# Performance work log

Measured on AMD Instinct MI355X. Metric: run time of the kernel, lower is better.

The kernel has to match this reference:

```python
import jax, jax.numpy as jnp
import numpy as np
import math

B, S, H = 2, 2048, 1024
NH, HD = 16, 64
MAX_SCALE = 4


def setup_inputs() -> dict:
    key = jax.random.key(0)
    ks = jax.random.split(key, 8)
    s = 0.02
    return {
        "x": jax.random.normal(ks[0], (B, S, H), dtype=jnp.float32),
        "Wqkv": jax.random.normal(ks[1], (H, 3 * H), dtype=jnp.float32) * s,
        "bqkv": jnp.zeros((3 * H,), dtype=jnp.float32),
        "Wout": jax.random.normal(ks[2], (H, H), dtype=jnp.float32) * s,
        "bout": jnp.zeros((H,), dtype=jnp.float32),
        "Wscale": jax.random.normal(ks[3], (H, MAX_SCALE), dtype=jnp.float32) * s,
        "bscale": jnp.zeros((MAX_SCALE,), dtype=jnp.float32),
    }


def reference(x, Wqkv, bqkv, Wout, bout, Wscale, bscale):
    b, s, h = x.shape
    inv_sqrt_hd = 1.0 / math.sqrt(HD)
    # qkv projection -> [3, b, nh, s, hd]
    qkv = (x @ Wqkv + bqkv).reshape(b, s, 3, NH, HD).transpose(2, 0, 3, 1, 4)
    q, k, v = qkv[0], qkv[1], qkv[2]
    # per-token soft weights over scales [b, s, max_scale]
    scale_weights = jax.nn.softmax(x @ Wscale + bscale, axis=-1)
    out = jnp.zeros((b, NH, s, HD), dtype=x.dtype)
    for scale_idx in range(MAX_SCALE):
        dilation = 2 ** scale_idx
        kd = k[:, :, ::dilation]  # strided (dilated) gather of keys
        vd = v[:, :, ::dilation]
        scores = jnp.einsum("bhqd,bhkd->bhqk", q, kd) * inv_sqrt_hd
        attn = jax.nn.softmax(scores, axis=-1)
        o = jnp.einsum("bhqk,bhkd->bhqd", attn, vd)
        w = scale_weights[:, :, scale_idx][:, None, :, None]  # [b,1,s,1]
        out = out + o * w
    out = out.transpose(0, 2, 1, 3).reshape(b, s, h)
    return out @ Wout + bout
```

## Files before the change

kernel.cpp:

```cpp
#include <hip/hip_runtime.h>
#include <stdint.h>

typedef unsigned short u16;
typedef __attribute__((ext_vector_type(8))) __bf16 bf8v;
typedef __attribute__((ext_vector_type(4))) float f4v;
typedef __attribute__((ext_vector_type(16))) float f16v;
typedef __attribute__((ext_vector_type(4))) uint32_t u32x4;

#define BB 2
#define SS 2048
#define HH 1024

#define OFF_Q   0u
#define OFF_K0  8388608u
#define OFF_V0  24117248u
#define OFF_V1  32505856u
#define OFF_V2  36700160u
#define OFF_V3  38797312u
#define OFF_WQT 39845888u
#define OFF_WOT 46137344u
#define OFF_XB  48234496u
#define OFF_SCW 56623104u

__device__ __forceinline__ u16 f2bf(float f) {
    union { float f; uint32_t u; } v; v.f = f;
    uint32_t r = v.u + 0x7fffu + ((v.u >> 16) & 1u);
    return (u16)(r >> 16);
}
__device__ __forceinline__ uint32_t pk2(float a, float b) {
    return (uint32_t)f2bf(a) | ((uint32_t)f2bf(b) << 16);
}
__device__ __forceinline__ uint32_t pkt2(float a, float b) {
    union { float f; uint32_t u; } x, y; x.f = a; y.f = b;
    return (x.u >> 16) | (y.u & 0xffff0000u);
}

__global__ __launch_bounds__(256) void xconv_kernel(const float* __restrict__ x,
                                                    u16* __restrict__ xb) {
    size_t t = (size_t)blockIdx.x * 256 + threadIdx.x;
    float4 v = *(const float4*)&x[t * 4];
    uint2 pk; pk.x = pk2(v.x, v.y); pk.y = pk2(v.z, v.w);
    *(uint2*)&xb[t * 4] = pk;
}

__global__ __launch_bounds__(256) void wconv_kernel(const float* __restrict__ W,
                                                    u16* __restrict__ Wt,
                                                    int N, int K) {
    __shared__ float tile[64][69];
    const int tid = threadIdx.x;
    const int n0 = blockIdx.x * 64, k0 = blockIdx.y * 64;
    const int r = tid >> 4, c4 = (tid & 15) * 4;
#pragma unroll
    for (int it = 0; it < 4; it++) {
        float4 v = *(const float4*)&W[(size_t)(k0 + it * 16 + r) * N + n0 + c4];
        tile[it * 16 + r][c4 + 0] = v.x; tile[it * 16 + r][c4 + 1] = v.y;
        tile[it * 16 + r][c4 + 2] = v.z; tile[it * 16 + r][c4 + 3] = v.w;
    }
    __syncthreads();
#pragma unroll
    for (int it = 0; it < 4; it++) {
        int n = it * 16 + r;
        uint2 pk;
        pk.x = pk2(tile[c4 + 0][n], tile[c4 + 1][n]);
        pk.y = pk2(tile[c4 + 2][n], tile[c4 + 3][n]);
        *(uint2*)&Wt[(size_t)(n0 + n) * K + k0 + c4] = pk;
    }
}

__global__ __launch_bounds__(256) void scale_kernel(const float* __restrict__ x,
                                                    const float* __restrict__ Wscale,
                                                    const float* __restrict__ bscale,
                                                    float* __restrict__ scw) {
    const int lane = threadIdx.x & 63;
    const int wid  = threadIdx.x >> 6;
    const int row  = blockIdx.x * 4 + wid;
    float a0 = 0.f, a1 = 0.f, a2 = 0.f, a3 = 0.f;
    for (int i = 0; i < 16; i++) {
        int hh = lane + i * 64;
        float xs = x[(size_t)row * HH + hh];
        float4 wv = *(const float4*)&Wscale[hh * 4];
        a0 += xs * wv.x; a1 += xs * wv.y; a2 += xs * wv.z; a3 += xs * wv.w;
    }
    for (int off = 1; off < 64; off <<= 1) {
        a0 += __shfl_xor(a0, off); a1 += __shfl_xor(a1, off);
        a2 += __shfl_xor(a2, off); a3 += __shfl_xor(a3, off);
    }
    if (lane == 0) {
        a0 += bscale[0]; a1 += bscale[1]; a2 += bscale[2]; a3 += bscale[3];
        float mx = fmaxf(fmaxf(a0, a1), fmaxf(a2, a3));
        float e0 = __expf(a0 - mx), e1 = __expf(a1 - mx);
        float e2 = __expf(a2 - mx), e3 = __expf(a3 - mx);
        float inv = 1.f / (e0 + e1 + e2 + e3);
        float4 o = {e0 * inv, e1 * inv, e2 * inv, e3 * inv};
        *(float4*)&scw[(size_t)row * 4] = o;
    }
}

template<int MODE>
__global__ __launch_bounds__(256) void gemm_bt(const u16* __restrict__ A,
                                               const u16* __restrict__ Bt,
                                               const float* __restrict__ bias,
                                               void* __restrict__ Cp,
                                               int N, int K) {
    __shared__ __align__(16) u16 At[128 * 40];
    __shared__ __align__(16) u16 Btl[128 * 40];
    const int tid  = threadIdx.x;
    const int lane = tid & 63;
    const int wid  = tid >> 6;
    const int l15  = lane & 15;
    const int quad = lane >> 4;
    const int wm = wid & 1, wn = wid >> 1;
    const int m0 = blockIdx.y * 128;
    const int n0 = blockIdx.x * 128;
    const int srow = tid >> 2;
    const int sc8  = (tid & 3) * 8;

    f4v acc[4][4];
#pragma unroll
    for (int i = 0; i < 4; i++)
#pragma unroll
        for (int j = 0; j < 4; j++) acc[i][j] = (f4v){0.f, 0.f, 0.f, 0.f};

    uint4 pa0 = *(const uint4*)(A  + (size_t)(m0 + srow) * K + sc8);
    uint4 pa1 = *(const uint4*)(A  + (size_t)(m0 + srow + 64) * K + sc8);
    uint4 pb0 = *(const uint4*)(Bt + (size_t)(n0 + srow) * K + sc8);
    uint4 pb1 = *(const uint4*)(Bt + (size_t)(n0 + srow + 64) * K + sc8);

    for (int kc = 0; kc < K; kc += 32) {
        __syncthreads();
        *(uint4*)&At[srow * 40 + sc8]         = pa0;
        *(uint4*)&At[(srow + 64) * 40 + sc8]  = pa1;
        *(uint4*)&Btl[srow * 40 + sc8]        = pb0;
        *(uint4*)&Btl[(srow + 64) * 40 + sc8] = pb1;
        __syncthreads();
        if (kc + 32 < K) {
            pa0 = *(const uint4*)(A  + (size_t)(m0 + srow) * K + kc + 32 + sc8);
            pa1 = *(const uint4*)(A  + (size_t)(m0 + srow + 64) * K + kc + 32 + sc8);
            pb0 = *(const uint4*)(Bt + (size_t)(n0 + srow) * K + kc + 32 + sc8);
            pb1 = *(const uint4*)(Bt + (size_t)(n0 + srow + 64) * K + kc + 32 + sc8);
        }
        bf8v af[4], bf[4];
#pragma unroll
        for (int t = 0; t < 4; t++) {
            af[t] = *(const bf8v*)&At[(wm * 64 + t * 16 + l15) * 40 + quad * 8];
            bf[t] = *(const bf8v*)&Btl[(wn * 64 + t * 16 + l15) * 40 + quad * 8];
        }
#pragma unroll
        for (int ti = 0; ti < 4; ti++)
#pragma unroll
            for (int tj = 0; tj < 4; tj++)
                acc[ti][tj] = __builtin_amdgcn_mfma_f32_16x16x32_bf16(af[ti], bf[tj], acc[ti][tj], 0, 0, 0);
    }

    if (MODE == 0) {
#pragma unroll
        for (int ti = 0; ti < 4; ti++)
#pragma unroll
            for (int tj = 0; tj < 4; tj++)
#pragma unroll
                for (int r = 0; r < 4; r++) {
                    int m = m0 + wm * 64 + ti * 16 + quad * 4 + r;
                    int n = n0 + wn * 64 + tj * 16 + l15;
                    ((float*)Cp)[(size_t)m * N + n] = acc[ti][tj][r] + bias[n];
                }
    } else {
        char* ws = (char*)Cp;
        u16* Qd = (u16*)ws;
        u16* K0 = (u16*)(ws + OFF_K0);
        u16* V0 = (u16*)(ws + OFF_V0); u16* V1 = (u16*)(ws + OFF_V1);
        u16* V2 = (u16*)(ws + OFF_V2); u16* V3 = (u16*)(ws + OFF_V3);
        const int region = n0 >> 10;
        if (region == 0) {
#pragma unroll
            for (int ti = 0; ti < 4; ti++)
#pragma unroll
                for (int tj = 0; tj < 4; tj++)
#pragma unroll
                    for (int r = 0; r < 4; r++) {
                        int m = m0 + wm * 64 + ti * 16 + quad * 4 + r;
                        int n = n0 + wn * 64 + tj * 16 + l15;
                        Qd[(size_t)m * 1024 + n] = f2bf(acc[ti][tj][r] + bias[n]);
                    }
        } else if (region == 1) {
#pragma unroll
            for (int ti = 0; ti < 4; ti++)
#pragma unroll
                for (int tj = 0; tj < 4; tj++) {
                    int n  = n0 + wn * 64 + tj * 16 + l15;
                    int nk = n - 1024;
                    int h = nk >> 6, hd = nk & 63;
#pragma unroll
                    for (int r = 0; r < 4; r++) {
                        int m = m0 + wm * 64 + ti * 16 + quad * 4 + r;
                        int bb = m >> 11, tok = m & 2047;
                        int bh = bb * 16 + h;
                        u16 bv = f2bf((acc[ti][tj][r] + bias[n]) * 0.18033688f);
                        K0[((size_t)bh * 2048 + tok) * 64 + hd] = bv;
                    }
                }
        } else {
#pragma unroll
            for (int ti = 0; ti < 4; ti++)
#pragma unroll
                for (int tj = 0; tj < 4; tj++) {
                    int n  = n0 + wn * 64 + tj * 16 + l15;
                    int nv = n - 2048;
                    int h = nv >> 6, hd = nv & 63;
                    int tokb = m0 + wm * 64 + ti * 16 + quad * 4;
                    int bb = tokb >> 11, tok = tokb & 2047;
                    int bh = bb * 16 + h;
                    float v0 = acc[ti][tj][0] + bias[n];
                    float v1 = acc[ti][tj][1] + bias[n];
                    float v2 = acc[ti][tj][2] + bias[n];
                    float v3 = acc[ti][tj][3] + bias[n];
                    u16 c0 = f2bf(v0), c1 = f2bf(v1), c2 = f2bf(v2), c3 = f2bf(v3);
                    uint2 pk;
                    pk.x = (uint32_t)c0 | ((uint32_t)c1 << 16);
                    pk.y = (uint32_t)c2 | ((uint32_t)c3 << 16);
                    int tokp = (tok & ~15) | ((tok & 4) << 1) | ((tok & 8) >> 1);
                    *(uint2*)&V0[((size_t)bh * 64 + hd) * 2048 + tokp] = pk;
                    int kk = tok >> 1;
                    int v1p = (kk & ~15) | ((kk & 2) << 2) | ((kk & 12) >> 1);
                    *(uint32_t*)&V1[((size_t)bh * 64 + hd) * 1024 + v1p] =
                        (uint32_t)c0 | ((uint32_t)c2 << 16);
                    int t2 = tok >> 2;
                    int v2i = (t2 & ~15) | ((t2 & 1) << 3) | ((t2 & 15) >> 1);
                    V2[((size_t)bh * 64 + hd) * 512 + v2i] = c0;
                    if (!(quad & 1)) V3[((size_t)bh * 64 + hd) * 256 + (tok >> 3)] = c0;
                }
        }
    }
}

__global__ __launch_bounds__(256, 2) void attn_kernel(const char* __restrict__ ws) {
    __shared__ __align__(16) u16 smem[15872];
    u16* Kt0  = smem;
    u16* Kt1  = smem + 2304;
    u16* Vt0  = smem + 4608;
    u16* Vt1  = smem + 7168;
    u16* V1t0 = smem + 9728;
    u16* V1t1 = smem + 11264;
    u16* V2t  = smem + 12800;
    u16* V3t  = smem + 14336;

    const u16* Qd    = (const u16*)(ws + OFF_Q);
    const float* scw = (const float*)(ws + OFF_SCW);
    u16* attnb       = (u16*)(ws + OFF_Q);

    const int tid  = threadIdx.x;
    const int lane = tid & 63;
    const int wid  = tid >> 6;
    const int l31  = lane & 31;
    const int half = lane >> 5;
    const int b = blockIdx.z, h = blockIdx.y;
    const int q  = blockIdx.x * 128 + wid * 32 + l31;
    const int bh = b * 16 + h;

    const int skey = tid >> 3;
    const int shd8 = (tid & 7) * 8;
    const int svhd = tid >> 2;
    const int svk8 = (tid & 3) * 8;
    const int vi4  = (tid & 3) * 4;

    bf8v qf[4];
#pragma unroll
    for (int ks = 0; ks < 4; ks++)
        qf[ks] = *(const bf8v*)(Qd + (size_t)(b * SS + q) * 1024 + h * 64 + ks * 16 + half * 8);

    const u16* Kb  = (const u16*)(ws + OFF_K0) + (size_t)bh * (2048 * 64);
    const u16* Vb0 = (const u16*)(ws + OFF_V0) + (size_t)bh * (64 * 2048);
    const u16* Vb1 = (const u16*)(ws + OFF_V1) + (size_t)bh * (64 * 1024);
    const u16* Vb2 = (const u16*)(ws + OFF_V2) + (size_t)bh * (64 * 512);
    const u16* Vb3 = (const u16*)(ws + OFF_V3) + (size_t)bh * (64 * 256);

    f16v oacc0[2], oacc1[2], oacc2[2], oacc3[2];
#pragma unroll
    for (int ht = 0; ht < 2; ht++)
#pragma unroll
        for (int r = 0; r < 16; r++) {
            oacc0[ht][r] = 0.f; oacc1[ht][r] = 0.f;
            oacc2[ht][r] = 0.f; oacc3[ht][r] = 0.f;
        }
    float ls0 = 0.f, ls1 = 0.f, ls2 = 0.f, ls3 = 0.f;

    uint4 kr  = *(const uint4*)(Kb + (size_t)skey * 64 + shd8);
    uint4 vr  = *(const uint4*)(Vb0 + (size_t)svhd * 2048 + svk8);
    uint2 v1r = *(const uint2*)(Vb1 + (size_t)svhd * 1024 + vi4);
    uint2 v2r = *(const uint2*)(Vb2 + (size_t)svhd * 512 + vi4);
    uint2 v3r = *(const uint2*)(Vb3 + (size_t)svhd * 256 + vi4);
    *(uint4*)&Kt0[skey * 72 + shd8] = kr;
    *(uint4*)&Vt0[svhd * 40 + svk8] = vr;
    *(uint2*)&V1t0[svhd * 24 + vi4] = v1r;
    kr  = *(const uint4*)(Kb + (size_t)(32 + skey) * 64 + shd8);
    vr  = *(const uint4*)(Vb0 + (size_t)svhd * 2048 + 32 + svk8);
    v1r = *(const uint2*)(Vb1 + (size_t)svhd * 1024 + 16 + vi4);
    __syncthreads();

    uint32_t Pa[4], Pb[4];
    union uu { u32x4 u; bf8v b; };

    for (int cc = 0; cc < 64; cc += 4) {
#pragma unroll
        for (int ph = 0; ph < 4; ph++) {
            const int c = cc + ph;
            u16* Ktc  = (ph & 1) ? Kt1 : Kt0;
            u16* Vtc  = (ph & 1) ? Vt1 : Vt0;
            u16* V1tc = (ph & 1) ? V1t1 : V1t0;
            u16* Ktn  = (ph & 1) ? Kt0 : Kt1;
            u16* Vtn  = (ph & 1) ? Vt0 : Vt1;
            u16* V1tn = (ph & 1) ? V1t0 : V1t1;

            f16v sa;
#pragma unroll
            for (int r = 0; r < 16; r++) sa[r] = 0.f;
#pragma unroll
            for (int ks = 0; ks < 4; ks++) {
                bf8v ka = *(const bf8v*)&Ktc[l31 * 72 + ks * 16 + half * 8];
                sa = __builtin_amdgcn_mfma_f32_32x32x16_bf16(ka, qf[ks], sa, 0, 0, 0);
            }
            float e[16];
#pragma unroll
            for (int g = 0; g < 4; g++) {
                float e0 = exp2f(sa[g * 4 + 0]);
                float e1 = exp2f(sa[g * 4 + 1]);
                float e2 = exp2f(sa[g * 4 + 2]);
                float e3 = exp2f(sa[g * 4 + 3]);
                e[g * 4 + 0] = e0; e[g * 4 + 1] = e1;
                e[g * 4 + 2] = e2; e[g * 4 + 3] = e3;
                ls0 += (e0 + e1) + (e2 + e3);
                ls1 += e0 + e2;
                ls2 += e0;
                if (!half) ls3 += e0;
            }
            uint32_t F00 = pkt2(e[0],  e[1]),  F01 = pkt2(e[2],  e[3]);
            uint32_t F02 = pkt2(e[4],  e[5]),  F03 = pkt2(e[6],  e[7]);
            uint32_t F10 = pkt2(e[8],  e[9]),  F11 = pkt2(e[10], e[11]);
            uint32_t F12 = pkt2(e[12], e[13]), F13 = pkt2(e[14], e[15]);
            uint32_t G0 = pkt2(e[0],  e[2]),   G1 = pkt2(e[4],  e[6]);
            uint32_t G2 = pkt2(e[8],  e[10]),  G3 = pkt2(e[12], e[14]);
            Pa[ph] = pkt2(e[0], e[4]);
            Pb[ph] = pkt2(e[8], e[12]);

            if (c + 1 < 64) {
                *(uint4*)&Ktn[skey * 72 + shd8] = kr;
                *(uint4*)&Vtn[svhd * 40 + svk8] = vr;
                *(uint2*)&V1tn[svhd * 24 + vi4] = v1r;
            }
            if (!(ph & 1)) {
                *(uint2*)&V2t[svhd * 24 + vi4] = v2r;
                if (ph == 0)
                    *(uint2*)&V3t[svhd * 24 + vi4] = v3r;
            }
            if (c + 2 < 64) {
                kr  = *(const uint4*)(Kb + (size_t)((c + 2) * 32 + skey) * 64 + shd8);
                vr  = *(const uint4*)(Vb0 + (size_t)svhd * 2048 + (c + 2) * 32 + svk8);
                v1r = *(const uint2*)(Vb1 + (size_t)svhd * 1024 + (c + 2) * 16 + vi4);
                if (!((c + 2) & 1))
                    v2r = *(const uint2*)(Vb2 + (size_t)svhd * 512 + (c + 2) * 8 + vi4);
                if (!((c + 2) & 3))
                    v3r = *(const uint2*)(Vb3 + (size_t)svhd * 256 + (c + 2) * 4 + vi4);
            }
            {
                uu p0; p0.u = (u32x4){F00, F01, F02, F03};
#pragma unroll
                for (int ht = 0; ht < 2; ht++) {
                    bf8v va = *(const bf8v*)&Vtc[(ht * 32 + l31) * 40 + half * 8];
                    oacc0[ht] = __builtin_amdgcn_mfma_f32_32x32x16_bf16(va, p0.b, oacc0[ht], 0, 0, 0);
                }
                uu p1; p1.u = (u32x4){F10, F11, F12, F13};
#pragma unroll
                for (int ht = 0; ht < 2; ht++) {
                    bf8v va = *(const bf8v*)&Vtc[(ht * 32 + l31) * 40 + 16 + half * 8];
                    oacc0[ht] = __builtin_amdgcn_mfma_f32_32x32x16_bf16(va, p1.b, oacc0[ht], 0, 0, 0);
                }
            }
            {
                uu ps; ps.u = (u32x4){G0, G1, G2, G3};
#pragma unroll
                for (int ht = 0; ht < 2; ht++) {
                    bf8v va1 = *(const bf8v*)&V1tc[(ht * 32 + l31) * 24 + half * 8];
                    oacc1[ht] = __builtin_amdgcn_mfma_f32_32x32x16_bf16(va1, ps.b, oacc1[ht], 0, 0, 0);
                }
            }
            if (ph == 1 || ph == 3) {
                uu p2; p2.u = (u32x4){Pa[ph - 1], Pb[ph - 1], Pa[ph], Pb[ph]};
#pragma unroll
                for (int ht = 0; ht < 2; ht++) {
                    bf8v va2 = *(const bf8v*)&V2t[(ht * 32 + l31) * 24 + half * 8];
                    oacc2[ht] = __builtin_amdgcn_mfma_f32_32x32x16_bf16(va2, p2.b, oacc2[ht], 0, 0, 0);
                }
            }
            if (ph == 3) {
                uint32_t t0 = __shfl_xor(Pa[2], 32);
                uint32_t t1 = __shfl_xor(Pb[2], 32);
                uint32_t t2 = __shfl_xor(Pa[3], 32);
                uint32_t t3 = __shfl_xor(Pb[3], 32);
                uint32_t w0 = half ? t0 : Pa[0];
                uint32_t w1 = half ? t1 : Pb[0];
                uint32_t w2 = half ? t2 : Pa[1];
                uint32_t w3 = half ? t3 : Pb[1];
                uu p3; p3.u = (u32x4){w0, w1, w2, w3};
#pragma unroll
                for (int ht = 0; ht < 2; ht++) {
                    bf8v va3 = *(const bf8v*)&V3t[(ht * 32 + l31) * 24 + half * 8];
                    oacc3[ht] = __builtin_amdgcn_mfma_f32_32x32x16_bf16(va3, p3.b, oacc3[ht], 0, 0, 0);
                }
            }
            __syncthreads();
        }
    }
    ls0 += __shfl_xor(ls0, 32);
    ls1 += __shfl_xor(ls1, 32);
    ls2 += __shfl_xor(ls2, 32);
    ls3 += __shfl_xor(ls3, 32);
    float4 sw = *(const float4*)&scw[(size_t)(b * SS + q) * 4];
    float w0 = sw.x / ls0, w1 = sw.y / ls1, w2 = sw.z / ls2, w3 = sw.w / ls3;

    const size_t base = (size_t)(b * SS + q) * 1024 + h * 64;
#pragma unroll
    for (int ht = 0; ht < 2; ht++)
#pragma unroll
        for (int g = 0; g < 4; g++) {
            float f0 = w0 * oacc0[ht][g * 4 + 0] + w1 * oacc1[ht][g * 4 + 0]
                     + w2 * oacc2[ht][g * 4 + 0] + w3 * oacc3[ht][g * 4 + 0];
            float f1 = w0 * oacc0[ht][g * 4 + 1] + w1 * oacc1[ht][g * 4 + 1]
                     + w2 * oacc2[ht][g * 4 + 1] + w3 * oacc3[ht][g * 4 + 1];
            float f2 = w0 * oacc0[ht][g * 4 + 2] + w1 * oacc1[ht][g * 4 + 2]
                     + w2 * oacc2[ht][g * 4 + 2] + w3 * oacc3[ht][g * 4 + 2];
            float f3 = w0 * oacc0[ht][g * 4 + 3] + w1 * oacc1[ht][g * 4 + 3]
                     + w2 * oacc2[ht][g * 4 + 3] + w3 * oacc3[ht][g * 4 + 3];
            uint2 pk;
            pk.x = pk2(f0, f1);
            pk.y = pk2(f2, f3);
            *(uint2*)&attnb[base + ht * 32 + g * 8 + half * 4] = pk;
        }
}

extern "C" void kernel_launch(void* const* d_in, const int* in_sizes, int n_in,
                              void* d_out, int out_size, void* d_ws, size_t ws_size,
                              hipStream_t stream) {
    const float* x      = (const float*)d_in[0];
    const float* Wqkv   = (const float*)d_in[1];
    const float* bqkv   = (const float*)d_in[2];
    const float* Wout   = (const float*)d_in[3];
    const float* bout   = (const float*)d_in[4];
    const float* Wscale = (const float*)d_in[5];
    const float* bscale = (const float*)d_in[6];
    float* out = (float*)d_out;

    char* ws = (char*)d_ws;
    u16*   wqt   = (u16*)(ws + OFF_WQT);
    u16*   wot   = (u16*)(ws + OFF_WOT);
    u16*   xb    = (u16*)(ws + OFF_XB);
    u16*   attnb = (u16*)(ws + OFF_Q);
    float* scw   = (float*)(ws + OFF_SCW);

    xconv_kernel<<<dim3(4096), dim3(256), 0, stream>>>(x, xb);
    wconv_kernel<<<dim3(48, 16), dim3(256), 0, stream>>>(Wqkv, wqt, 3072, 1024);
    wconv_kernel<<<dim3(16, 16), dim3(256), 0, stream>>>(Wout, wot, 1024, 1024);
    scale_kernel<<<dim3(1024), dim3(256), 0, stream>>>(x, Wscale, bscale, scw);
    gemm_bt<1><<<dim3(24, 32), dim3(256), 0, stream>>>(xb, wqt, bqkv, (void*)ws, 3072, 1024);
    attn_kernel<<<dim3(16, 16, 2), dim3(256), 0, stream>>>(ws);
    gemm_bt<0><<<dim3(8, 32), dim3(256), 0, stream>>>(attnb, wot, bout, (void*)out, 1024, 1024);
}
```

Measured before the change: 264.1 us.

## Software-pipeline QK and PV across chunks with deeper LDS buffering and XCD remap

Restructures the attention loop so the QK^T MFMAs for chunk c run while the exp/pack and PV MFMAs handle chunk c-1. This needs triple- and quad-buffered K/V tiles in LDS, which roughly doubles shared memory, and a drain step after the loop. It also remaps block indices so that blocks for the same batch/head land on the same XCD, to improve L2 reuse. The larger LDS footprint and the extra live score registers may lower occupancy.

```diff
diff --git a/kernel.cpp b/kernel.cpp
--- a/kernel.cpp
+++ b/kernel.cpp
@@ -232,16 +232,78 @@
     }
 }
 
+#define EXPPACK(sap, phf)                                                      \
+    {                                                                          \
+        float e[16];                                                           \
+        for (int g = 0; g < 4; g++) {                                          \
+            float x0 = exp2f((sap)[g * 4 + 0]);                                \
+            float x1 = exp2f((sap)[g * 4 + 1]);                                \
+            float x2 = exp2f((sap)[g * 4 + 2]);                                \
+            float x3 = exp2f((sap)[g * 4 + 3]);                                \
+            e[g * 4 + 0] = x0; e[g * 4 + 1] = x1;                              \
+            e[g * 4 + 2] = x2; e[g * 4 + 3] = x3;                              \
+            ls0 += (x0 + x1) + (x2 + x3);                                      \
+            ls1 += x0 + x2;                                                    \
+            ls2 += x0;                                                         \
+            if (!half) ls3 += x0;                                              \
+        }                                                                      \
+        F00 = pkt2(e[0],  e[1]);  F01 = pkt2(e[2],  e[3]);                     \
+        F02 = pkt2(e[4],  e[5]);  F03 = pkt2(e[6],  e[7]);                     \
+        F10 = pkt2(e[8],  e[9]);  F11 = pkt2(e[10], e[11]);                    \
+        F12 = pkt2(e[12], e[13]); F13 = pkt2(e[14], e[15]);                    \
+        G0  = pkt2(e[0],  e[2]);  G1  = pkt2(e[4],  e[6]);                     \
+        G2  = pkt2(e[8],  e[10]); G3  = pkt2(e[12], e[14]);                    \
+        Pa[(phf)] = pkt2(e[0], e[4]);                                          \
+        Pb[(phf)] = pkt2(e[8], e[12]);                                         \
+    }
+
+#define PVALL(v0p, v1p, v2p, v3p, phf, DO2, DO3)                               \
+    {                                                                          \
+        uu p0; p0.u = (u32x4){F00, F01, F02, F03};                             \
+        uu p1; p1.u = (u32x4){F10, F11, F12, F13};                             \
+        for (int ht = 0; ht < 2; ht++) {                                       \
+            bf8v va = *(const bf8v*)&(v0p)[(ht * 32 + l31) * 40 + half * 8];   \
+            oacc0[ht] = __builtin_amdgcn_mfma_f32_32x32x16_bf16(va, p0.b, oacc0[ht], 0, 0, 0); \
+            bf8v vb = *(const bf8v*)&(v0p)[(ht * 32 + l31) * 40 + 16 + half * 8]; \
+            oacc0[ht] = __builtin_amdgcn_mfma_f32_32x32x16_bf16(vb, p1.b, oacc0[ht], 0, 0, 0); \
+        }                                                                      \
+        uu ps; ps.u = (u32x4){G0, G1, G2, G3};                                 \
+        for (int ht = 0; ht < 2; ht++) {                                       \
+            bf8v va1 = *(const bf8v*)&(v1p)[(ht * 32 + l31) * 24 + half * 8];  \
+            oacc1[ht] = __builtin_amdgcn_mfma_f32_32x32x16_bf16(va1, ps.b, oacc1[ht], 0, 0, 0); \
+        }                                                                      \
+        if (DO2) {                                                             \
+            uu p2; p2.u = (u32x4){Pa[((phf) + 3) & 3], Pb[((phf) + 3) & 3],    \
+                                  Pa[(phf)], Pb[(phf)]};                       \
+            for (int ht = 0; ht < 2; ht++) {                                   \
+                bf8v va2 = *(const bf8v*)&(v2p)[(ht * 32 + l31) * 24 + half * 8]; \
+                oacc2[ht] = __builtin_amdgcn_mfma_f32_32x32x16_bf16(va2, p2.b, oacc2[ht], 0, 0, 0); \
+            }                                                                  \
+        }                                                                      \
+        if (DO3) {                                                             \
+            uint32_t t0 = __shfl_xor(Pa[2], 32);                               \
+            uint32_t t1 = __shfl_xor(Pb[2], 32);                               \
+            uint32_t t2 = __shfl_xor(Pa[3], 32);                               \
+            uint32_t t3 = __shfl_xor(Pb[3], 32);                               \
+            uint32_t w0 = half ? t0 : Pa[0];                                   \
+            uint32_t w1 = half ? t1 : Pb[0];                                   \
+            uint32_t w2 = half ? t2 : Pa[1];                                   \
+            uint32_t w3 = half ? t3 : Pb[1];                                   \
+            uu p3; p3.u = (u32x4){w0, w1, w2, w3};                             \
+            for (int ht = 0; ht < 2; ht++) {                                   \
+                bf8v va3 = *(const bf8v*)&(v3p)[(ht * 32 + l31) * 24 + half * 8]; \
+                oacc3[ht] = __builtin_amdgcn_mfma_f32_32x32x16_bf16(va3, p3.b, oacc3[ht], 0, 0, 0); \
+            }                                                                  \
+        }                                                                      \
+    }
+
 __global__ __launch_bounds__(256, 2) void attn_kernel(const char* __restrict__ ws) {
-    __shared__ __align__(16) u16 smem[15872];
-    u16* Kt0  = smem;
-    u16* Kt1  = smem + 2304;
-    u16* Vt0  = smem + 4608;
-    u16* Vt1  = smem + 7168;
-    u16* V1t0 = smem + 9728;
-    u16* V1t1 = smem + 11264;
-    u16* V2t  = smem + 12800;
-    u16* V3t  = smem + 14336;
+    __shared__ __align__(16) u16 smem[30976];
+    auto KtB = [&](int i) { return smem + i * 2304; };
+    auto VtB = [&](int i) { return smem + 6912 + i * 2560; };
+    auto V1B = [&](int i) { return smem + 17152 + i * 1536; };
+    auto V2B = [&](int i) { return smem + 23296 + i * 1536; };
+    auto V3B = [&](int i) { return smem + 27904 + i * 1536; };
 
     const u16* Qd    = (const u16*)(ws + OFF_Q);
     const float* scw = (const float*)(ws + OFF_SCW);
@@ -252,8 +314,13 @@
     const int wid  = tid >> 6;
     const int l31  = lane & 31;
     const int half = lane >> 5;
-    const int b = blockIdx.z, h = blockIdx.y;
-    const int q  = blockIdx.x * 128 + wid * 32 + l31;
+
+    const int f   = blockIdx.x + 16 * blockIdx.y + 256 * blockIdx.z;
+    const int xcd = f & 7, jj = f >> 3;
+    const int grp = xcd * 4 + (jj >> 4);
+    const int qt  = jj & 15;
+    const int b = grp >> 4, h = grp & 15;
+    const int q  = qt * 128 + wid * 32 + l31;
     const int bh = b * 16 + h;
 
     const int skey = tid >> 3;
@@ -283,131 +350,81 @@
         }
     float ls0 = 0.f, ls1 = 0.f, ls2 = 0.f, ls3 = 0.f;
 
-    uint4 kr  = *(const uint4*)(Kb + (size_t)skey * 64 + shd8);
-    uint4 vr  = *(const uint4*)(Vb0 + (size_t)svhd * 2048 + svk8);
-    uint2 v1r = *(const uint2*)(Vb1 + (size_t)svhd * 1024 + vi4);
-    uint2 v2r = *(const uint2*)(Vb2 + (size_t)svhd * 512 + vi4);
-    uint2 v3r = *(const uint2*)(Vb3 + (size_t)svhd * 256 + vi4);
-    *(uint4*)&Kt0[skey * 72 + shd8] = kr;
-    *(uint4*)&Vt0[svhd * 40 + svk8] = vr;
-    *(uint2*)&V1t0[svhd * 24 + vi4] = v1r;
-    kr  = *(const uint4*)(Kb + (size_t)(32 + skey) * 64 + shd8);
-    vr  = *(const uint4*)(Vb0 + (size_t)svhd * 2048 + 32 + svk8);
-    v1r = *(const uint2*)(Vb1 + (size_t)svhd * 1024 + 16 + vi4);
+#pragma unroll
+    for (int cN = 0; cN < 2; cN++) {
+        *(uint4*)&KtB(cN)[skey * 72 + shd8] =
+            *(const uint4*)(Kb + (size_t)(cN * 32 + skey) * 64 + shd8);
+        *(uint4*)&VtB(cN)[svhd * 40 + svk8] =
+            *(const uint4*)(Vb0 + (size_t)svhd * 2048 + cN * 32 + svk8);
+        *(uint2*)&V1B(cN)[svhd * 24 + vi4] =
+            *(const uint2*)(Vb1 + (size_t)svhd * 1024 + cN * 16 + vi4);
+    }
+    *(uint2*)&V2B(0)[svhd * 24 + vi4] = *(const uint2*)(Vb2 + (size_t)svhd * 512 + vi4);
+    *(uint2*)&V3B(0)[svhd * 24 + vi4] = *(const uint2*)(Vb3 + (size_t)svhd * 256 + vi4);
+    uint4 kr  = *(const uint4*)(Kb  + (size_t)(64 + skey) * 64 + shd8);
+    uint4 vr  = *(const uint4*)(Vb0 + (size_t)svhd * 2048 + 64 + svk8);
+    uint2 v1r = *(const uint2*)(Vb1 + (size_t)svhd * 1024 + 32 + vi4);
+    uint2 v2r = *(const uint2*)(Vb2 + (size_t)svhd * 512 + 16 + vi4);
+    uint2 v3r = {};
     __syncthreads();
 
     uint32_t Pa[4], Pb[4];
+    f16v sa0, sa1;
     union uu { u32x4 u; bf8v b; };
 
     for (int cc = 0; cc < 64; cc += 4) {
 #pragma unroll
         for (int ph = 0; ph < 4; ph++) {
             const int c = cc + ph;
-            u16* Ktc  = (ph & 1) ? Kt1 : Kt0;
-            u16* Vtc  = (ph & 1) ? Vt1 : Vt0;
-            u16* V1tc = (ph & 1) ? V1t1 : V1t0;
-            u16* Ktn  = (ph & 1) ? Kt0 : Kt1;
-            u16* Vtn  = (ph & 1) ? Vt0 : Vt1;
-            u16* V1tn = (ph & 1) ? V1t0 : V1t1;
-
-            f16v sa;
-#pragma unroll
-            for (int r = 0; r < 16; r++) sa[r] = 0.f;
-#pragma unroll
-            for (int ks = 0; ks < 4; ks++) {
-                bf8v ka = *(const bf8v*)&Ktc[l31 * 72 + ks * 16 + half * 8];
-                sa = __builtin_amdgcn_mfma_f32_32x32x16_bf16(ka, qf[ks], sa, 0, 0, 0);
+            const int phf = (ph + 3) & 3;
+            const bool dofin = (ph > 0) || (cc > 0);
+            uint32_t F00, F01, F02, F03, F10, F11, F12, F13, G0, G1, G2, G3;
+
+            f16v& sc = (ph & 1) ? sa1 : sa0;
+            const f16v& sp = (ph & 1) ? sa0 : sa1;
+#pragma unroll
+            for (int r = 0; r < 16; r++) sc[r] = 0.f;
+            {
+                u16* kt = KtB(c % 3);
+#pragma unroll
+                for (int ks = 0; ks < 4; ks++) {
+                    bf8v ka = *(const bf8v*)&kt[l31 * 72 + ks * 16 + half * 8];
+                    sc = __builtin_amdgcn_mfma_f32_32x32x16_bf16(ka, qf[ks], sc, 0, 0, 0);
+                }
             }
-            float e[16];
-#pragma unroll
-            for (int g = 0; g < 4; g++) {
-                float e0 = exp2f(sa[g * 4 + 0]);
-                float e1 = exp2f(sa[g * 4 + 1]);
-                float e2 = exp2f(sa[g * 4 + 2]);
-                float e3 = exp2f(sa[g * 4 + 3]);
-                e[g * 4 + 0] = e0; e[g * 4 + 1] = e1;
-                e[g * 4 + 2] = e2; e[g * 4 + 3] = e3;
-                ls0 += (e0 + e1) + (e2 + e3);
-                ls1 += e0 + e2;
-                ls2 += e0;
-                if (!half) ls3 += e0;
+            if (dofin) EXPPACK(sp, phf)
+            if (c + 2 < 64) {
+                *(uint4*)&KtB((c + 2) % 3)[skey * 72 + shd8] = kr;
+                *(uint4*)&VtB((ph + 2) & 3)[svhd * 40 + svk8] = vr;
+                *(uint2*)&V1B((ph + 2) & 3)[svhd * 24 + vi4] = v1r;
+                if (((c + 2) & 1) == 0) {
+                    *(uint2*)&V2B(((c + 2) >> 1) % 3)[svhd * 24 + vi4] = v2r;
+                    if (((c + 2) & 3) == 0)
+                        *(uint2*)&V3B(((c + 2) >> 2) & 1)[svhd * 24 + vi4] = v3r;
+                }
             }
-            uint32_t F00 = pkt2(e[0],  e[1]),  F01 = pkt2(e[2],  e[3]);
-            uint32_t F02 = pkt2(e[4],  e[5]),  F03 = pkt2(e[6],  e[7]);
-            uint32_t F10 = pkt2(e[8],  e[9]),  F11 = pkt2(e[10], e[11]);
-            uint32_t F12 = pkt2(e[12], e[13]), F13 = pkt2(e[14], e[15]);
-            uint32_t G0 = pkt2(e[0],  e[2]),   G1 = pkt2(e[4],  e[6]);
-            uint32_t G2 = pkt2(e[8],  e[10]),  G3 = pkt2(e[12], e[14]);
-            Pa[ph] = pkt2(e[0], e[4]);
-            Pb[ph] = pkt2(e[8], e[12]);
-
-            if (c + 1 < 64) {
-                *(uint4*)&Ktn[skey * 72 + shd8] = kr;
-                *(uint4*)&Vtn[svhd * 40 + svk8] = vr;
-                *(uint2*)&V1tn[svhd * 24 + vi4] = v1r;
+            if (c + 3 < 64) {
+                kr  = *(const uint4*)(Kb  + (size_t)((c + 3) * 32 + skey) * 64 + shd8);
+                vr  = *(const uint4*)(Vb0 + (size_t)svhd * 2048 + (c + 3) * 32 + svk8);
+                v1r = *(const uint2*)(Vb1 + (size_t)svhd * 1024 + (c + 3) * 16 + vi4);
+                if (((c + 3) & 1) == 0) {
+                    v2r = *(const uint2*)(Vb2 + (size_t)svhd * 512 + (c + 3) * 8 + vi4);
+                    if (((c + 3) & 3) == 0)
+                        v3r = *(const uint2*)(Vb3 + (size_t)svhd * 256 + (c + 3) * 4 + vi4);
+                }
             }
-            if (!(ph & 1)) {
-                *(uint2*)&V2t[svhd * 24 + vi4] = v2r;
-                if (ph == 0)
-                    *(uint2*)&V3t[svhd * 24 + vi4] = v3r;
-            }
-            if (c + 2 < 64) {
-                kr  = *(const uint4*)(Kb + (size_t)((c + 2) * 32 + skey) * 64 + shd8);
-                vr  = *(const uint4*)(Vb0 + (size_t)svhd * 2048 + (c + 2) * 32 + svk8);
-                v1r = *(const uint2*)(Vb1 + (size_t)svhd * 1024 + (c + 2) * 16 + vi4);
-                if (!((c + 2) & 1))
-                    v2r = *(const uint2*)(Vb2 + (size_t)svhd * 512 + (c + 2) * 8 + vi4);
-                if (!((c + 2) & 3))
-                    v3r = *(const uint2*)(Vb3 + (size_t)svhd * 256 + (c + 2) * 4 + vi4);
-            }
-            {
-                uu p0; p0.u = (u32x4){F00, F01, F02, F03};
-#pragma unroll
-                for (int ht = 0; ht < 2; ht++) {
-                    bf8v va = *(const bf8v*)&Vtc[(ht * 32 + l31) * 40 + half * 8];
-                    oacc0[ht] = __builtin_amdgcn_mfma_f32_32x32x16_bf16(va, p0.b, oacc0[ht], 0, 0, 0);
-                }
-                uu p1; p1.u = (u32x4){F10, F11, F12, F13};
-#pragma unroll
-                for (int ht = 0; ht < 2; ht++) {
-                    bf8v va = *(const bf8v*)&Vtc[(ht * 32 + l31) * 40 + 16 + half * 8];
-                    oacc0[ht] = __builtin_amdgcn_mfma_f32_32x32x16_bf16(va, p1.b, oacc0[ht], 0, 0, 0);
-                }
-            }
-            {
-                uu ps; ps.u = (u32x4){G0, G1, G2, G3};
-#pragma unroll
-                for (int ht = 0; ht < 2; ht++) {
-                    bf8v va1 = *(const bf8v*)&V1tc[(ht * 32 + l31) * 24 + half * 8];
-                    oacc1[ht] = __builtin_amdgcn_mfma_f32_32x32x16_bf16(va1, ps.b, oacc1[ht], 0, 0, 0);
-                }
-            }
-            if (ph == 1 || ph == 3) {
-                uu p2; p2.u = (u32x4){Pa[ph - 1], Pb[ph - 1], Pa[ph], Pb[ph]};
-#pragma unroll
-                for (int ht = 0; ht < 2; ht++) {
-                    bf8v va2 = *(const bf8v*)&V2t[(ht * 32 + l31) * 24 + half * 8];
-                    oacc2[ht] = __builtin_amdgcn_mfma_f32_32x32x16_bf16(va2, p2.b, oacc2[ht], 0, 0, 0);
-                }
-            }
-            if (ph == 3) {
-                uint32_t t0 = __shfl_xor(Pa[2], 32);
-                uint32_t t1 = __shfl_xor(Pb[2], 32);
-                uint32_t t2 = __shfl_xor(Pa[3], 32);
-                uint32_t t3 = __shfl_xor(Pb[3], 32);
-                uint32_t w0 = half ? t0 : Pa[0];
-                uint32_t w1 = half ? t1 : Pb[0];
-                uint32_t w2 = half ? t2 : Pa[1];
-                uint32_t w3 = half ? t3 : Pb[1];
-                uu p3; p3.u = (u32x4){w0, w1, w2, w3};
-#pragma unroll
-                for (int ht = 0; ht < 2; ht++) {
-                    bf8v va3 = *(const bf8v*)&V3t[(ht * 32 + l31) * 24 + half * 8];
-                    oacc3[ht] = __builtin_amdgcn_mfma_f32_32x32x16_bf16(va3, p3.b, oacc3[ht], 0, 0, 0);
-                }
-            }
+            if (dofin)
+                PVALL(VtB((ph + 3) & 3), V1B((ph + 3) & 3),
+                      V2B(((c - 2) >> 1) % 3), V3B(((c - 4) >> 2) & 1),
+                      phf, (phf == 1 || phf == 3), (phf == 3))
             __syncthreads();
         }
+    }
+    {
+        const f16v& sp = sa1;
+        uint32_t F00, F01, F02, F03, F10, F11, F12, F13, G0, G1, G2, G3;
+        EXPPACK(sp, 3)
+        PVALL(VtB(3), V1B(3), V2B(1), V3B(1), 3, true, true)
     }
     ls0 += __shfl_xor(ls0, 32);
     ls1 += __shfl_xor(ls1, 32);
```

Measured after the change: 312.5 us. 1.18x slower.

## Use direct global-to-LDS loads in GEMM and XCD-aware block remap in attention

Applied to the files above, without the earlier changes.

The GEMM staging path now loads global memory straight into LDS through global_load_lds, so the register prefetch and LDS store instructions go away. The LDS tile is unpadded (stride 32) to match the layout those direct loads write. The register double-buffer prefetch is removed, so load latency is no longer hidden behind the MFMA work, and the unpadded stride may cause LDS bank conflicts. The attention kernel also remaps block indices so that all query tiles of a (batch, head) group land on the same XCD, which should improve L2 reuse of K/V.

```diff
diff --git a/kernel.cpp b/kernel.cpp
--- a/kernel.cpp
+++ b/kernel.cpp
@@ -33,6 +33,12 @@
 __device__ __forceinline__ uint32_t pkt2(float a, float b) {
     union { float f; uint32_t u; } x, y; x.f = a; y.f = b;
     return (x.u >> 16) | (y.u & 0xffff0000u);
+}
+
+__device__ __forceinline__ void gl2lds16(const u16* g, u16* l) {
+    __builtin_amdgcn_global_load_lds(
+        (__attribute__((address_space(1))) void*)g,
+        (__attribute__((address_space(3))) void*)l, 16, 0, 0);
 }
 
 __global__ __launch_bounds__(256) void xconv_kernel(const float* __restrict__ x,
@@ -102,8 +108,8 @@
                                                const float* __restrict__ bias,
                                                void* __restrict__ Cp,
                                                int N, int K) {
-    __shared__ __align__(16) u16 At[128 * 40];
-    __shared__ __align__(16) u16 Btl[128 * 40];
+    __shared__ __align__(16) u16 At[128 * 32];
+    __shared__ __align__(16) u16 Btl[128 * 32];
     const int tid  = threadIdx.x;
     const int lane = tid & 63;
     const int wid  = tid >> 6;
@@ -112,38 +118,28 @@
     const int wm = wid & 1, wn = wid >> 1;
     const int m0 = blockIdx.y * 128;
     const int n0 = blockIdx.x * 128;
-    const int srow = tid >> 2;
-    const int sc8  = (tid & 3) * 8;
+    const int cA0 = wid * 2, cA1 = wid * 2 + 1;
+    const int lrow = lane >> 2;
+    const int lcol = (lane & 3) * 8;
 
     f4v acc[4][4];
 #pragma unroll
     for (int i = 0; i < 4; i++)
 #pragma unroll
         for (int j = 0; j < 4; j++) acc[i][j] = (f4v){0.f, 0.f, 0.f, 0.f};
-
-    uint4 pa0 = *(const uint4*)(A  + (size_t)(m0 + srow) * K + sc8);
-    uint4 pa1 = *(const uint4*)(A  + (size_t)(m0 + srow + 64) * K + sc8);
-    uint4 pb0 = *(const uint4*)(Bt + (size_t)(n0 + srow) * K + sc8);
-    uint4 pb1 = *(const uint4*)(Bt + (size_t)(n0 + srow + 64) * K + sc8);
 
     for (int kc = 0; kc < K; kc += 32) {
         __syncthreads();
-        *(uint4*)&At[srow * 40 + sc8]         = pa0;
-        *(uint4*)&At[(srow + 64) * 40 + sc8]  = pa1;
-        *(uint4*)&Btl[srow * 40 + sc8]        = pb0;
-        *(uint4*)&Btl[(srow + 64) * 40 + sc8] = pb1;
+        gl2lds16(A  + (size_t)(m0 + cA0 * 16 + lrow) * K + kc + lcol, At  + cA0 * 512);
+        gl2lds16(A  + (size_t)(m0 + cA1 * 16 + lrow) * K + kc + lcol, At  + cA1 * 512);
+        gl2lds16(Bt + (size_t)(n0 + cA0 * 16 + lrow) * K + kc + lcol, Btl + cA0 * 512);
+        gl2lds16(Bt + (size_t)(n0 + cA1 * 16 + lrow) * K + kc + lcol, Btl + cA1 * 512);
         __syncthreads();
-        if (kc + 32 < K) {
-            pa0 = *(const uint4*)(A  + (size_t)(m0 + srow) * K + kc + 32 + sc8);
-            pa1 = *(const uint4*)(A  + (size_t)(m0 + srow + 64) * K + kc + 32 + sc8);
-            pb0 = *(const uint4*)(Bt + (size_t)(n0 + srow) * K + kc + 32 + sc8);
-            pb1 = *(const uint4*)(Bt + (size_t)(n0 + srow + 64) * K + kc + 32 + sc8);
-        }
         bf8v af[4], bf[4];
 #pragma unroll
         for (int t = 0; t < 4; t++) {
-            af[t] = *(const bf8v*)&At[(wm * 64 + t * 16 + l15) * 40 + quad * 8];
-            bf[t] = *(const bf8v*)&Btl[(wn * 64 + t * 16 + l15) * 40 + quad * 8];
+            af[t] = *(const bf8v*)&At[(wm * 64 + t * 16 + l15) * 32 + quad * 8];
+            bf[t] = *(const bf8v*)&Btl[(wn * 64 + t * 16 + l15) * 32 + quad * 8];
         }
 #pragma unroll
         for (int ti = 0; ti < 4; ti++)
@@ -252,8 +248,13 @@
     const int wid  = tid >> 6;
     const int l31  = lane & 31;
     const int half = lane >> 5;
-    const int b = blockIdx.z, h = blockIdx.y;
-    const int q  = blockIdx.x * 128 + wid * 32 + l31;
+
+    const int f   = blockIdx.x + 16 * blockIdx.y + 256 * blockIdx.z;
+    const int xcd = f & 7, fj = f >> 3;
+    const int grp = xcd * 4 + (fj >> 4);
+    const int qt  = fj & 15;
+    const int b = grp >> 4, h = grp & 15;
+    const int q  = qt * 128 + wid * 32 + l31;
     const int bh = b * 16 + h;
 
     const int skey = tid >> 3;
```

Measured after the change: 268.7 us. No clear change (+1.7%).
